# Optimization experiments

Measured on AMD Instinct MI355X. Metric: run time of the kernel, lower is better.

## Reference

```python
import jax, jax.numpy as jnp
import numpy as np

# 24 directional shifts (dy, dx): out[h,w] = in[h-dy, w-dx], zero elsewhere.
SHIFTS = [(0,1),(0,-1),(1,0),(-1,0),(1,1),(-1,-1),(1,-1),(-1,1),
          (0,2),(0,-2),(2,0),(-2,0),(2,2),(-2,-2),(2,-2),(-2,2),
          (2,1),(1,2),(2,-1),(1,-2),(-2,1),(-1,2),(-2,-1),(-1,-2)]

def shift2d(xg, dy, dx):
    B, G, H, W = xg.shape
    pt, pb = max(dy,0), max(-dy,0)
    pl, pr = max(dx,0), max(-dx,0)
    xp = jnp.pad(xg, ((0,0),(0,0),(pt,pb),(pl,pr)))
    return xp[:, :, pb:pb+H, pr:pr+W]

def mul_shift(x4, gamma=1.0/24.0):
    B, C, H, W = x4.shape
    g = int(C * gamma)
    parts = [shift2d(x4[:, i*g:(i+1)*g], dy, dx) for i, (dy, dx) in enumerate(SHIFTS)]
    parts.append(x4[:, 24*g:])
    return jnp.concatenate(parts, axis=1)

def zigzag_indices(h, w, start='top-left', direction='horizontal'):
    if start == 'top-left':   row_start, col_start, row_step, col_step = 0, 0, 1, 1
    elif start == 'top-right': row_start, col_start, row_step, col_step = 0, w-1, 1, -1
    elif start == 'bottom-left': row_start, col_start, row_step, col_step = h-1, 0, -1, 1
    else:                     row_start, col_start, row_step, col_step = h-1, w-1, -1, -1
    idx = []
    for i in range(h):
        r = row_start + row_step * i
        if direction == 'horizontal':
            cols = range(w) if r % 2 == 0 else range(w-1, -1, -1)
            idx += [r * w + c for c in cols]
        else:
            cc = col_start + col_step * i
            rows = range(h) if cc % 2 == 0 else range(h-1, -1, -1)
            idx += [rr * w + cc for rr in rows]
    return np.asarray(idx, dtype=np.int32)

def wkv(w, u, k, v):
    """Numerically stable RWKV WKV recurrence. w,u:(C,) k,v:(B,T,C) -> (B,T,C)."""
    B, T, C = k.shape
    def step(carry, kv):
        p, q, o = carry
        kt, vt = kv
        no = jnp.maximum(o, u + kt)
        A = jnp.exp(o - no); Bc = jnp.exp(u + kt - no)
        y = (A * p + Bc * vt) / (A * q + Bc)
        no2 = jnp.maximum(w + o, kt)
        A2 = jnp.exp(w + o - no2); B2 = jnp.exp(kt - no2)
        return (A2 * p + B2 * vt, A2 * q + B2, no2), y
    init = (jnp.zeros((B, C), k.dtype), jnp.zeros((B, C), k.dtype),
            jnp.full((B, C), -1e38, k.dtype))
    _, ys = jax.lax.scan(step, init, (jnp.swapaxes(k, 0, 1), jnp.swapaxes(v, 0, 1)))
    return jnp.swapaxes(ys, 0, 1)

def setup_inputs() -> dict:
    key = jax.random.key(0)
    ks = jax.random.split(key, 8)
    B, H, W, C = 8, 64, 64, 768
    scale = 0.02
    return {
        'x': jax.random.normal(ks[0], (B, H*W, C), jnp.float32),
        'key_w': jax.random.normal(ks[1], (C, C), jnp.float32) * scale,
        'value_w': jax.random.normal(ks[2], (C, C), jnp.float32) * scale,
        'receptance_w': jax.random.normal(ks[3], (C, C), jnp.float32) * scale,
        'output_w': jax.random.normal(ks[4], (C, C), jnp.float32) * scale,
        'spatial_decay': jax.random.normal(ks[5], (2, C), jnp.float32),
        'spatial_first': jax.random.normal(ks[6], (2, C), jnp.float32),
        'h': H, 'w': W,
    }

def reference(x, key_w, value_w, receptance_w, output_w, spatial_decay, spatial_first, h, w):
    B, T, C = x.shape
    # layer_id=0 -> scheme ('top-left','horizontal')
    order = jnp.asarray(zigzag_indices(h, w, 'top-left', 'horizontal'))
    inv = jnp.argsort(order)
    # jit_func: mul_shift in (B,C,H,W), zigzag reorder along T, projections
    x4 = jnp.transpose(x.reshape(B, h, w, C), (0, 3, 1, 2))
    x4 = mul_shift(x4)
    xs = jnp.transpose(x4.reshape(B, C, T)[:, :, order], (0, 2, 1))  # (B,T,C)
    k = xs @ key_w.T
    v = xs @ value_w.T
    sr = jax.nn.sigmoid(xs @ receptance_w.T)
    # recurrence j=0
    v = wkv(spatial_decay[0] / T, spatial_first[0] / T, k, v)
    # recurrence j=1: zigzag-permute, WKV, inverse-permute (horizontal -> same grid)
    k2 = k[:, order]
    v2 = v[:, order]
    v2 = wkv(spatial_decay[1] / T, spatial_first[1] / T, k2, v2)
    v = v2[:, inv]
    return (sr * v) @ output_w.T
```

## Files before the change

### kernel.cpp

```cpp
#include <hip/hip_runtime.h>
#include <hip/hip_bf16.h>
#include <hip/hip_fp16.h>

#define T_SEQ 4096
#define CDIM  768
#define BDIM  8
#define MROWS (BDIM * T_SEQ)
#define NKVR  (3 * CDIM)
#define CHL   32
#define NCH   (T_SEQ / CHL)
#define BC    (BDIM * CDIM)

typedef __attribute__((ext_vector_type(8))) short   short8;
typedef __attribute__((ext_vector_type(4))) float   floatx4;
typedef unsigned short ushort_t;
typedef unsigned int   uint_t;
struct ushort4_t { ushort_t x, y, z, w; };

__device__ __forceinline__ ushort_t f2b(float f) {
    __hip_bfloat16 h = __float2bfloat16(f);
    return *(ushort_t*)&h;
}
__device__ __forceinline__ float b2f(ushort_t s) {
    __hip_bfloat16 h;
    *(ushort_t*)&h = s;
    return __bfloat162float(h);
}
__device__ __forceinline__ ushort_t f2h(float f) {
    __half h = __float2half(f);
    return *(ushort_t*)&h;
}
__device__ __forceinline__ float h2f(ushort_t s) {
    __half h;
    *(ushort_t*)&h = s;
    return __half2float(h);
}

__device__ __forceinline__ void gload_lds16(const void* g, void* l) {
    __builtin_amdgcn_global_load_lds(
        (const __attribute__((address_space(1))) void*)g,
        (__attribute__((address_space(3))) void*)l, 16, 0, 0);
}

__constant__ int c_dy[24] = {0,0,1,-1,1,-1,1,-1,0,0,2,-2,2,-2,2,-2,2,1,2,1,-2,-1,-2,-1};
__constant__ int c_dx[24] = {1,-1,0,0,1,-1,-1,1,2,-2,0,0,2,-2,-2,2,1,2,-1,-2,1,2,-1,-2};

__global__ void cvt_weights(const float* __restrict__ kw, const float* __restrict__ vw,
                            const float* __restrict__ rw, const float* __restrict__ ow,
                            ushort_t* __restrict__ wkvr, ushort_t* __restrict__ wo) {
    int i = blockIdx.x * 256 + threadIdx.x;
    if (i < CDIM * CDIM) {
        wkvr[i]                   = f2b(kw[i]);
        wkvr[i + CDIM * CDIM]     = f2b(vw[i]);
        wkvr[i + 2 * CDIM * CDIM] = f2b(rw[i]);
        wo[i]                     = f2b(ow[i]);
    }
}

__global__ void shift_zigzag(const float* __restrict__ x, ushort_t* __restrict__ xs) {
    size_t i = (size_t)blockIdx.x * 256 + threadIdx.x;
    if (i >= (size_t)MROWS * (CDIM / 4)) return;
    int c4 = (int)(i % (CDIM / 4)) * 4;
    size_t bt = i / (CDIM / 4);
    int tz = (int)(bt % T_SEQ);
    int b  = (int)(bt / T_SEQ);
    int r = tz >> 6, pos = tz & 63;
    int xcol = (r & 1) ? (63 - pos) : pos;
    int g = c4 >> 5;
    int ys = r - c_dy[g];
    int xsrc = xcol - c_dx[g];
    float4 val = {0.f, 0.f, 0.f, 0.f};
    if ((unsigned)ys < 64u && (unsigned)xsrc < 64u)
        val = *(const float4*)(x + ((size_t)b * T_SEQ + (size_t)(ys * 64 + xsrc)) * CDIM + c4);
    ushort4_t o;
    o.x = f2b(val.x); o.y = f2b(val.y); o.z = f2b(val.z); o.w = f2b(val.w);
    *(ushort4_t*)(xs + bt * CDIM + c4) = o;
}

template <int MODE, int NB>
__global__ __launch_bounds__(256, 3) void gemm_bt(
    const ushort_t* __restrict__ A, const ushort_t* __restrict__ Bw,
    ushort_t* __restrict__ kbuf, ushort_t* __restrict__ vbuf,
    ushort_t* __restrict__ out_sr, float* __restrict__ out_f) {
    __shared__ ushort_t As[128 * 64];
    __shared__ ushort_t Bs[128 * 64];
    const int p    = blockIdx.x;
    const int xcd  = p & 7;
    const int s    = p >> 3;
    const int mb   = xcd + 8 * (s / NB);
    const int nb   = s % NB;
    const int m0   = mb * 128;
    const int n0   = nb * 128;
    const int t    = threadIdx.x;
    const int lane = t & 63;
    const int wv   = t >> 6;
    const int wm   = (wv & 1) * 64;
    const int wn   = (wv >> 1) * 64;
    const int srow = t >> 3;
    const int sch  = t & 7;
    const int l15  = lane & 15;
    const int l4   = lane >> 4;

    floatx4 acc[4][4];
#pragma unroll
    for (int i = 0; i < 4; i++)
#pragma unroll
        for (int j = 0; j < 4; j++) acc[i][j] = (floatx4){0.f, 0.f, 0.f, 0.f};

    for (int kk = 0; kk < CDIM; kk += 64) {
        __syncthreads();
#pragma unroll
        for (int j = 0; j < 4; j++) {
            const int rowA = 32 * j + srow;
            const int gc   = sch ^ (rowA & 7);
            gload_lds16(A  + (size_t)(m0 + rowA) * CDIM + kk + gc * 8,
                        (void*)(As + j * 2048 + t * 8));
            gload_lds16(Bw + (size_t)(n0 + rowA) * CDIM + kk + gc * 8,
                        (void*)(Bs + j * 2048 + t * 8));
        }
        __syncthreads();
#pragma unroll
        for (int k2 = 0; k2 < 2; k2++) {
            short8 af[4], bfv[4];
#pragma unroll
            for (int mi = 0; mi < 4; mi++) {
                int ra = wm + mi * 16 + l15;
                int c  = k2 * 4 + l4;
                af[mi] = *(const short8*)(As + ra * 64 + ((c ^ (ra & 7)) << 3));
            }
#pragma unroll
            for (int ni = 0; ni < 4; ni++) {
                int rb = wn + ni * 16 + l15;
                int c  = k2 * 4 + l4;
                bfv[ni] = *(const short8*)(Bs + rb * 64 + ((c ^ (rb & 7)) << 3));
            }
#pragma unroll
            for (int mi = 0; mi < 4; mi++)
#pragma unroll
                for (int ni = 0; ni < 4; ni++)
                    acc[mi][ni] = __builtin_amdgcn_mfma_f32_16x16x32_bf16(
                        af[mi], bfv[ni], acc[mi][ni], 0, 0, 0);
        }
    }

    const int region = (MODE == 0) ? (nb / 6) : 0;
    const int ncb = n0 - region * CDIM;
#pragma unroll
    for (int mi = 0; mi < 4; mi++) {
#pragma unroll
        for (int ni = 0; ni < 4; ni++) {
            int nc = ncb + wn + ni * 16 + l15;
#pragma unroll
            for (int r = 0; r < 4; r++) {
                int mg = m0 + wm + mi * 16 + l4 * 4 + r;
                float val = acc[mi][ni][r];
                if (MODE == 0) {
                    if (region == 0)
                        kbuf[(size_t)mg * CDIM + nc] = f2h(val);
                    else if (region == 1)
                        vbuf[(size_t)mg * CDIM + nc] = f2h(val);
                    else
                        out_sr[(size_t)mg * CDIM + nc] =
                            f2b(1.0f / (1.0f + __expf(-val)));
                } else {
                    out_f[(size_t)mg * CDIM + (n0 + wn + ni * 16 + l15)] = val;
                }
            }
        }
    }
}


__global__ __launch_bounds__(256) void wkv_chunk_sum0(
    const ushort_t* __restrict__ kb, const ushort_t* __restrict__ vb,
    const float* __restrict__ sd,
    float* __restrict__ sumP, float* __restrict__ sumQ, float* __restrict__ sumO) {
    int gid = blockIdx.x * 256 + threadIdx.x;
    int bc = gid % BC;
    int ch = gid / BC;
    int b = bc / CDIM, c = bc % CDIM;
    const float w = sd[c] * (1.0f / (float)T_SEQ);
    const size_t base = ((size_t)b * T_SEQ + ch * CHL) * CDIM + c;
    const ushort_t* kp = kb + base;
    const ushort_t* vp = vb + base;
    float p = 0.f, q = 0.f, o = -1e38f;
#pragma unroll 8
    for (int i = 0; i < CHL; i++) {
        float kt = h2f(kp[(size_t)i * CDIM]), vt = h2f(vp[(size_t)i * CDIM]);
        float wo_ = w + o;
        float no2 = fmaxf(wo_, kt);
        float A2 = __expf(wo_ - no2), B2 = __expf(kt - no2);
        p = A2 * p + B2 * vt;
        q = A2 * q + B2;
        o = no2;
    }
    size_t idx = (size_t)ch * BC + bc;
    sumP[idx] = p; sumQ[idx] = q; sumO[idx] = o;
}

__global__ __launch_bounds__(256) void wkv_chunk_scan(
    const float* __restrict__ sumP, const float* __restrict__ sumQ,
    const float* __restrict__ sumO,
    float* __restrict__ inP, float* __restrict__ inQ, float* __restrict__ inO,
    const float* __restrict__ sd, int pass) {
    int bc = blockIdx.x * 256 + threadIdx.x;
    if (bc >= BC) return;
    int c = bc % CDIM;
    const float w = sd[pass * CDIM + c] * (1.0f / (float)T_SEQ);
    const float Lw = w * (float)CHL;
    float p = 0.f, q = 0.f, o = -1e38f;
    for (int ch = 0; ch < NCH; ch++) {
        size_t idx = (size_t)ch * BC + bc;
        inP[idx] = p; inQ[idx] = q; inO[idx] = o;
        float Pc = sumP[idx], Qc = sumQ[idx], Oc = sumO[idx];
        float ow_ = o + Lw;
        float no = fmaxf(ow_, Oc);
        float e1 = __expf(ow_ - no), e2 = __expf(Oc - no);
        p = e1 * p + e2 * Pc;
        q = e1 * q + e2 * Qc;
        o = no;
    }
}

__global__ __launch_bounds__(256) void wkv_replay0_sum1(
    const ushort_t* __restrict__ kb, ushort_t* __restrict__ vb,
    const float* __restrict__ sd, const float* __restrict__ sf,
    const float* __restrict__ inP, const float* __restrict__ inQ,
    const float* __restrict__ inO,
    float* __restrict__ sumP, float* __restrict__ sumQ, float* __restrict__ sumO) {
    int gid = blockIdx.x * 256 + threadIdx.x;
    int bc = gid % BC;
    int ch = gid / BC;
    int b = bc / CDIM, c = bc % CDIM;
    const float w1 = sd[c] * (1.0f / (float)T_SEQ);
    const float u1 = sf[c] * (1.0f / (float)T_SEQ);
    const size_t base = ((size_t)b * T_SEQ + ch * CHL) * CDIM + c;
    const ushort_t* kp = kb + base;
    ushort_t* vp = vb + base;
    size_t idx = (size_t)ch * BC + bc;
    float p = inP[idx], q = inQ[idx], o = inO[idx];
    float yv[CHL];
    float kvk[CHL];
#pragma unroll
    for (int i = 0; i < CHL; i++) {
        float kt = h2f(kp[(size_t)i * CDIM]), vt = h2f(vp[(size_t)i * CDIM]);
        kvk[i] = kt;
        float uk = u1 + kt;
        float no = fmaxf(o, uk);
        float Ae = __expf(o - no), Be = __expf(uk - no);
        float y = (Ae * p + Be * vt) / (Ae * q + Be);
        float wo_ = w1 + o;
        float no2 = fmaxf(wo_, kt);
        float A2 = __expf(wo_ - no2), B2 = __expf(kt - no2);
        p = A2 * p + B2 * vt;
        q = A2 * q + B2;
        o = no2;
        yv[i] = y;
        vp[(size_t)i * CDIM] = f2h(y);
    }
    const float w2 = sd[CDIM + c] * (1.0f / (float)T_SEQ);
    float p2 = 0.f, q2 = 0.f, o2 = -1e38f;
    const bool rev = (ch >> 1) & 1;
#pragma unroll
    for (int j = 0; j < CHL; j++) {
        int i = rev ? (CHL - 1 - j) : j;
        float kt = kvk[i], vt = yv[i];
        float wo_ = w2 + o2;
        float no2 = fmaxf(wo_, kt);
        float A2 = __expf(wo_ - no2), B2 = __expf(kt - no2);
        p2 = A2 * p2 + B2 * vt;
        q2 = A2 * q2 + B2;
        o2 = no2;
    }
    size_t idx2 = (size_t)((ch & 2) ? (ch ^ 1) : ch) * BC + bc;
    sumP[idx2] = p2; sumQ[idx2] = q2; sumO[idx2] = o2;
}

__global__ __launch_bounds__(256) void wkv_replay1(
    const ushort_t* __restrict__ kb, const ushort_t* __restrict__ vb,
    const ushort_t* __restrict__ srb, ushort_t* __restrict__ a2,
    const float* __restrict__ sd, const float* __restrict__ sf,
    const float* __restrict__ inP, const float* __restrict__ inQ,
    const float* __restrict__ inO) {
    int gid = blockIdx.x * 256 + threadIdx.x;
    int bc = gid % BC;
    int ch = gid / BC;
    int b = bc / CDIM, c = bc % CDIM;
    const float w = sd[CDIM + c] * (1.0f / (float)T_SEQ);
    const float u = sf[CDIM + c] * (1.0f / (float)T_SEQ);
    size_t base = (size_t)b * T_SEQ * CDIM + c;
    size_t idx = (size_t)ch * BC + bc;
    float p = inP[idx], q = inQ[idx], o = inO[idx];
    const int r = ch >> 1;
    const int pos0 = (ch & 1) * CHL;
#pragma unroll 8
    for (int i = 0; i < CHL; i++) {
        int pos = pos0 + i;
        int col = (r & 1) ? (63 - pos) : pos;
        size_t off = base + (size_t)(r * 64 + col) * CDIM;
        float kt = h2f(kb[off]), vt = h2f(vb[off]);
        float uk = u + kt;
        float no = fmaxf(o, uk);
        float Ae = __expf(o - no), Be = __expf(uk - no);
        float y = (Ae * p + Be * vt) / (Ae * q + Be);
        float wo_ = w + o;
        float no2 = fmaxf(wo_, kt);
        float A2 = __expf(wo_ - no2), B2 = __expf(kt - no2);
        p = A2 * p + B2 * vt;
        q = A2 * q + B2;
        o = no2;
        a2[off] = f2b(y * b2f(srb[off]));
    }
}

extern "C" void kernel_launch(void* const* d_in, const int* in_sizes, int n_in,
                              void* d_out, int out_size, void* d_ws, size_t ws_size,
                              hipStream_t stream) {
    (void)in_sizes; (void)n_in; (void)out_size; (void)ws_size;
    const float* x  = (const float*)d_in[0];
    const float* kw = (const float*)d_in[1];
    const float* vw = (const float*)d_in[2];
    const float* rw = (const float*)d_in[3];
    const float* ow = (const float*)d_in[4];
    const float* sd = (const float*)d_in[5];
    const float* sf = (const float*)d_in[6];
    float* out = (float*)d_out;

    char* ws = (char*)d_ws;
    size_t off = 0;
    auto alloc = [&](size_t bytes) -> void* {
        void* p = ws + off;
        off += (bytes + 255) & ~(size_t)255;
        return p;
    };
    ushort_t* xs   = (ushort_t*)alloc((size_t)MROWS * CDIM * 2);
    ushort_t* kb   = (ushort_t*)alloc((size_t)MROWS * CDIM * 2);
    ushort_t* vb   = (ushort_t*)alloc((size_t)MROWS * CDIM * 2);
    ushort_t* srb  = (ushort_t*)alloc((size_t)MROWS * CDIM * 2);
    ushort_t* wkvr = (ushort_t*)alloc((size_t)NKVR * CDIM * 2);
    ushort_t* wo   = (ushort_t*)alloc((size_t)CDIM * CDIM * 2);
    float*    sumP = (float*)   alloc((size_t)NCH * BC * 4);
    float*    sumQ = (float*)   alloc((size_t)NCH * BC * 4);
    float*    sumO = (float*)   alloc((size_t)NCH * BC * 4);
    float*    inP  = (float*)   alloc((size_t)NCH * BC * 4);
    float*    inQ  = (float*)   alloc((size_t)NCH * BC * 4);
    float*    inO  = (float*)   alloc((size_t)NCH * BC * 4);

    cvt_weights<<<(CDIM * CDIM + 255) / 256, 256, 0, stream>>>(kw, vw, rw, ow, wkvr, wo);
    shift_zigzag<<<(int)(((size_t)MROWS * (CDIM / 4) + 255) / 256), 256, 0, stream>>>(x, xs);
    gemm_bt<0, 18><<<(MROWS / 128) * (NKVR / 128), 256, 0, stream>>>(
        xs, wkvr, kb, vb, srb, nullptr);

    const int nwkv = NCH * BC;
    wkv_chunk_sum0<<<nwkv / 256, 256, 0, stream>>>(kb, vb, sd, sumP, sumQ, sumO);
    wkv_chunk_scan<<<(BC + 255) / 256, 256, 0, stream>>>(sumP, sumQ, sumO,
                                                         inP, inQ, inO, sd, 0);
    wkv_replay0_sum1<<<nwkv / 256, 256, 0, stream>>>(kb, vb, sd, sf,
                                                     inP, inQ, inO, sumP, sumQ, sumO);
    wkv_chunk_scan<<<(BC + 255) / 256, 256, 0, stream>>>(sumP, sumQ, sumO,
                                                         inP, inQ, inO, sd, 1);
    wkv_replay1<<<nwkv / 256, 256, 0, stream>>>(kb, vb, srb, xs,
                                                sd, sf, inP, inQ, inO);

    gemm_bt<1, 6><<<(MROWS / 128) * (CDIM / 128), 256, 0, stream>>>(
        xs, wo, nullptr, nullptr, nullptr, out);
}
```

Baseline: 566.6 us.

## Store k/v/sr in channel-major layout for vectorized contiguous WKV chunk access

The first GEMM now writes the k, v and sigmoid(r) planes transposed as (B, C, T), packing four consecutive time steps per store. This lets every WKV chunk kernel load its 32-step chunk with wide short8 loads instead of strided per-element reads. The chunk-summary buffers become channel-major too, and the shift kernel now handles 8 channels per thread. The cost is strided transposed stores in the GEMM epilogue and more registers in the fully unrolled WKV kernels.

```diff
diff --git a/kernel.cpp b/kernel.cpp
--- a/kernel.cpp
+++ b/kernel.cpp
@@ -15,7 +15,6 @@
 typedef __attribute__((ext_vector_type(4))) float   floatx4;
 typedef unsigned short ushort_t;
 typedef unsigned int   uint_t;
-struct ushort4_t { ushort_t x, y, z, w; };
 
 __device__ __forceinline__ ushort_t f2b(float f) {
     __hip_bfloat16 h = __float2bfloat16(f);
@@ -59,29 +58,34 @@
 
 __global__ void shift_zigzag(const float* __restrict__ x, ushort_t* __restrict__ xs) {
     size_t i = (size_t)blockIdx.x * 256 + threadIdx.x;
-    if (i >= (size_t)MROWS * (CDIM / 4)) return;
-    int c4 = (int)(i % (CDIM / 4)) * 4;
-    size_t bt = i / (CDIM / 4);
+    int c8 = (int)(i % (CDIM / 8)) * 8;
+    size_t bt = i / (CDIM / 8);
     int tz = (int)(bt % T_SEQ);
     int b  = (int)(bt / T_SEQ);
     int r = tz >> 6, pos = tz & 63;
     int xcol = (r & 1) ? (63 - pos) : pos;
-    int g = c4 >> 5;
+    int g = c8 >> 5;
     int ys = r - c_dy[g];
     int xsrc = xcol - c_dx[g];
-    float4 val = {0.f, 0.f, 0.f, 0.f};
-    if ((unsigned)ys < 64u && (unsigned)xsrc < 64u)
-        val = *(const float4*)(x + ((size_t)b * T_SEQ + (size_t)(ys * 64 + xsrc)) * CDIM + c4);
-    ushort4_t o;
-    o.x = f2b(val.x); o.y = f2b(val.y); o.z = f2b(val.z); o.w = f2b(val.w);
-    *(ushort4_t*)(xs + bt * CDIM + c4) = o;
+    float4 v0 = {0.f, 0.f, 0.f, 0.f}, v1 = {0.f, 0.f, 0.f, 0.f};
+    if ((unsigned)ys < 64u && (unsigned)xsrc < 64u) {
+        const float* src = x + ((size_t)b * T_SEQ + (size_t)(ys * 64 + xsrc)) * CDIM + c8;
+        v0 = *(const float4*)(src);
+        v1 = *(const float4*)(src + 4);
+    }
+    short8 o;
+    o[0] = (short)f2b(v0.x); o[1] = (short)f2b(v0.y);
+    o[2] = (short)f2b(v0.z); o[3] = (short)f2b(v0.w);
+    o[4] = (short)f2b(v1.x); o[5] = (short)f2b(v1.y);
+    o[6] = (short)f2b(v1.z); o[7] = (short)f2b(v1.w);
+    *(short8*)(xs + bt * CDIM + c8) = o;
 }
 
 template <int MODE, int NB>
-__global__ __launch_bounds__(256, 3) void gemm_bt(
+__device__ __forceinline__ void gemm_body(
     const ushort_t* __restrict__ A, const ushort_t* __restrict__ Bw,
     ushort_t* __restrict__ kbuf, ushort_t* __restrict__ vbuf,
-    ushort_t* __restrict__ out_sr, float* __restrict__ out_f) {
+    ushort_t* __restrict__ srbuf, float* __restrict__ out_f) {
     __shared__ ushort_t As[128 * 64];
     __shared__ ushort_t Bs[128 * 64];
     const int p    = blockIdx.x;
@@ -143,31 +147,59 @@
         }
     }
 
-    const int region = (MODE == 0) ? (nb / 6) : 0;
-    const int ncb = n0 - region * CDIM;
-#pragma unroll
-    for (int mi = 0; mi < 4; mi++) {
-#pragma unroll
-        for (int ni = 0; ni < 4; ni++) {
-            int nc = ncb + wn + ni * 16 + l15;
-#pragma unroll
-            for (int r = 0; r < 4; r++) {
-                int mg = m0 + wm + mi * 16 + l4 * 4 + r;
-                float val = acc[mi][ni][r];
-                if (MODE == 0) {
-                    if (region == 0)
-                        kbuf[(size_t)mg * CDIM + nc] = f2h(val);
-                    else if (region == 1)
-                        vbuf[(size_t)mg * CDIM + nc] = f2h(val);
-                    else
-                        out_sr[(size_t)mg * CDIM + nc] =
-                            f2b(1.0f / (1.0f + __expf(-val)));
+    if (MODE == 0) {
+        const int region = nb / 6;
+        const int ncb = n0 - region * CDIM;
+        const int bidx = mb >> 5;
+        const int tt   = (mb & 31) * 128;
+        ushort_t* plane = (region == 0) ? kbuf : (region == 1) ? vbuf : srbuf;
+#pragma unroll
+        for (int mi = 0; mi < 4; mi++) {
+#pragma unroll
+            for (int ni = 0; ni < 4; ni++) {
+                const int nc = ncb + wn + ni * 16 + l15;
+                const int t0 = tt + wm + mi * 16 + l4 * 4;
+                uint_t lo, hi;
+                if (region == 2) {
+                    lo = (uint_t)f2b(1.0f / (1.0f + __expf(-acc[mi][ni][0]))) |
+                         ((uint_t)f2b(1.0f / (1.0f + __expf(-acc[mi][ni][1]))) << 16);
+                    hi = (uint_t)f2b(1.0f / (1.0f + __expf(-acc[mi][ni][2]))) |
+                         ((uint_t)f2b(1.0f / (1.0f + __expf(-acc[mi][ni][3]))) << 16);
                 } else {
-                    out_f[(size_t)mg * CDIM + (n0 + wn + ni * 16 + l15)] = val;
+                    lo = (uint_t)f2h(acc[mi][ni][0]) | ((uint_t)f2h(acc[mi][ni][1]) << 16);
+                    hi = (uint_t)f2h(acc[mi][ni][2]) | ((uint_t)f2h(acc[mi][ni][3]) << 16);
+                }
+                uint2 pk = make_uint2(lo, hi);
+                *(uint2*)(plane + ((size_t)bidx * CDIM + nc) * T_SEQ + t0) = pk;
+            }
+        }
+    } else {
+#pragma unroll
+        for (int mi = 0; mi < 4; mi++) {
+#pragma unroll
+            for (int ni = 0; ni < 4; ni++) {
+                const int nc = n0 + wn + ni * 16 + l15;
+#pragma unroll
+                for (int r = 0; r < 4; r++) {
+                    const int mg = m0 + wm + mi * 16 + l4 * 4 + r;
+                    out_f[(size_t)mg * CDIM + nc] = acc[mi][ni][r];
                 }
             }
         }
     }
+}
+
+__global__ __launch_bounds__(256, 3) void gemm_kvr(
+    const ushort_t* __restrict__ A, const ushort_t* __restrict__ Bw,
+    ushort_t* __restrict__ kbuf, ushort_t* __restrict__ vbuf,
+    ushort_t* __restrict__ srbuf) {
+    gemm_body<0, 18>(A, Bw, kbuf, vbuf, srbuf, nullptr);
+}
+
+__global__ __launch_bounds__(256, 3) void gemm_out(
+    const ushort_t* __restrict__ A, const ushort_t* __restrict__ Bw,
+    float* __restrict__ out_f) {
+    gemm_body<1, 6>(A, Bw, nullptr, nullptr, nullptr, out_f);
 }
 
 
@@ -176,17 +208,20 @@
     const float* __restrict__ sd,
     float* __restrict__ sumP, float* __restrict__ sumQ, float* __restrict__ sumO) {
     int gid = blockIdx.x * 256 + threadIdx.x;
-    int bc = gid % BC;
-    int ch = gid / BC;
-    int b = bc / CDIM, c = bc % CDIM;
+    int ch = gid & (NCH - 1);
+    int bc = gid >> 7;
+    int c = bc % CDIM;
     const float w = sd[c] * (1.0f / (float)T_SEQ);
-    const size_t base = ((size_t)b * T_SEQ + ch * CHL) * CDIM + c;
-    const ushort_t* kp = kb + base;
-    const ushort_t* vp = vb + base;
+    const short8* kp = (const short8*)(kb + (size_t)bc * T_SEQ + ch * CHL);
+    const short8* vp = (const short8*)(vb + (size_t)bc * T_SEQ + ch * CHL);
+    short8 ks[4], vs[4];
+#pragma unroll
+    for (int r = 0; r < 4; r++) { ks[r] = kp[r]; vs[r] = vp[r]; }
     float p = 0.f, q = 0.f, o = -1e38f;
-#pragma unroll 8
+#pragma unroll
     for (int i = 0; i < CHL; i++) {
-        float kt = h2f(kp[(size_t)i * CDIM]), vt = h2f(vp[(size_t)i * CDIM]);
+        float kt = h2f((ushort_t)ks[i >> 3][i & 7]);
+        float vt = h2f((ushort_t)vs[i >> 3][i & 7]);
         float wo_ = w + o;
         float no2 = fmaxf(wo_, kt);
         float A2 = __expf(wo_ - no2), B2 = __expf(kt - no2);
@@ -194,7 +229,7 @@
         q = A2 * q + B2;
         o = no2;
     }
-    size_t idx = (size_t)ch * BC + bc;
+    size_t idx = (size_t)bc * NCH + ch;
     sumP[idx] = p; sumQ[idx] = q; sumO[idx] = o;
 }
 
@@ -208,11 +243,17 @@
     int c = bc % CDIM;
     const float w = sd[pass * CDIM + c] * (1.0f / (float)T_SEQ);
     const float Lw = w * (float)CHL;
+    const float* sp = sumP + (size_t)bc * NCH;
+    const float* sq = sumQ + (size_t)bc * NCH;
+    const float* so = sumO + (size_t)bc * NCH;
+    float* ip = inP + (size_t)bc * NCH;
+    float* iq = inQ + (size_t)bc * NCH;
+    float* io = inO + (size_t)bc * NCH;
     float p = 0.f, q = 0.f, o = -1e38f;
+#pragma unroll 4
     for (int ch = 0; ch < NCH; ch++) {
-        size_t idx = (size_t)ch * BC + bc;
-        inP[idx] = p; inQ[idx] = q; inO[idx] = o;
-        float Pc = sumP[idx], Qc = sumQ[idx], Oc = sumO[idx];
+        ip[ch] = p; iq[ch] = q; io[ch] = o;
+        float Pc = sp[ch], Qc = sq[ch], Oc = so[ch];
         float ow_ = o + Lw;
         float no = fmaxf(ow_, Oc);
         float e1 = __expf(ow_ - no), e2 = __expf(Oc - no);
@@ -231,20 +272,21 @@
     int gid = blockIdx.x * 256 + threadIdx.x;
     int bc = gid % BC;
     int ch = gid / BC;
-    int b = bc / CDIM, c = bc % CDIM;
+    int c = bc % CDIM;
     const float w1 = sd[c] * (1.0f / (float)T_SEQ);
     const float u1 = sf[c] * (1.0f / (float)T_SEQ);
-    const size_t base = ((size_t)b * T_SEQ + ch * CHL) * CDIM + c;
-    const ushort_t* kp = kb + base;
-    ushort_t* vp = vb + base;
-    size_t idx = (size_t)ch * BC + bc;
-    float p = inP[idx], q = inQ[idx], o = inO[idx];
-    float yv[CHL];
-    float kvk[CHL];
+    const size_t base = (size_t)bc * T_SEQ + ch * CHL;
+    const short8* kp = (const short8*)(kb + base);
+    short8* vp = (short8*)(vb + base);
+    short8 ks[4], vs[4], ys[4];
+#pragma unroll
+    for (int r = 0; r < 4; r++) { ks[r] = kp[r]; vs[r] = vp[r]; }
+    size_t sidx = (size_t)bc * NCH + ch;
+    float p = inP[sidx], q = inQ[sidx], o = inO[sidx];
 #pragma unroll
     for (int i = 0; i < CHL; i++) {
-        float kt = h2f(kp[(size_t)i * CDIM]), vt = h2f(vp[(size_t)i * CDIM]);
-        kvk[i] = kt;
+        float kt = h2f((ushort_t)ks[i >> 3][i & 7]);
+        float vt = h2f((ushort_t)vs[i >> 3][i & 7]);
         float uk = u1 + kt;
         float no = fmaxf(o, uk);
         float Ae = __expf(o - no), Be = __expf(uk - no);
@@ -255,25 +297,34 @@
         p = A2 * p + B2 * vt;
         q = A2 * q + B2;
         o = no2;
-        yv[i] = y;
-        vp[(size_t)i * CDIM] = f2h(y);
-    }
+        ys[i >> 3][i & 7] = (short)f2h(y);
+    }
+#pragma unroll
+    for (int r = 0; r < 4; r++) vp[r] = ys[r];
     const float w2 = sd[CDIM + c] * (1.0f / (float)T_SEQ);
     float p2 = 0.f, q2 = 0.f, o2 = -1e38f;
-    const bool rev = (ch >> 1) & 1;
-#pragma unroll
-    for (int j = 0; j < CHL; j++) {
-        int i = rev ? (CHL - 1 - j) : j;
-        float kt = kvk[i], vt = yv[i];
-        float wo_ = w2 + o2;
-        float no2 = fmaxf(wo_, kt);
-        float A2 = __expf(wo_ - no2), B2 = __expf(kt - no2);
-        p2 = A2 * p2 + B2 * vt;
-        q2 = A2 * q2 + B2;
-        o2 = no2;
-    }
-    size_t idx2 = (size_t)((ch & 2) ? (ch ^ 1) : ch) * BC + bc;
-    sumP[idx2] = p2; sumQ[idx2] = q2; sumO[idx2] = o2;
+#define P2STEP(IDX)                                                         \
+    {                                                                       \
+        float kt = h2f((ushort_t)ks[(IDX) >> 3][(IDX) & 7]);                \
+        float yt = h2f((ushort_t)ys[(IDX) >> 3][(IDX) & 7]);                \
+        float wo_ = w2 + o2;                                                \
+        float nn = fmaxf(wo_, kt);                                          \
+        float A2 = __expf(wo_ - nn), B2 = __expf(kt - nn);                  \
+        p2 = A2 * p2 + B2 * yt;                                             \
+        q2 = A2 * q2 + B2;                                                  \
+        o2 = nn;                                                            \
+    }
+    if (((ch >> 1) & 1) == 0) {
+#pragma unroll
+        for (int j = 0; j < CHL; j++) P2STEP(j)
+    } else {
+#pragma unroll
+        for (int j = 0; j < CHL; j++) P2STEP(CHL - 1 - j)
+    }
+#undef P2STEP
+    int idx2 = (ch & 2) ? (ch ^ 1) : ch;
+    size_t oidx = (size_t)bc * NCH + idx2;
+    sumP[oidx] = p2; sumQ[oidx] = q2; sumO[oidx] = o2;
 }
 
 __global__ __launch_bounds__(256) void wkv_replay1(
@@ -288,29 +339,44 @@
     int b = bc / CDIM, c = bc % CDIM;
     const float w = sd[CDIM + c] * (1.0f / (float)T_SEQ);
     const float u = sf[CDIM + c] * (1.0f / (float)T_SEQ);
-    size_t base = (size_t)b * T_SEQ * CDIM + c;
-    size_t idx = (size_t)ch * BC + bc;
-    float p = inP[idx], q = inQ[idx], o = inO[idx];
     const int r = ch >> 1;
     const int pos0 = (ch & 1) * CHL;
-#pragma unroll 8
-    for (int i = 0; i < CHL; i++) {
-        int pos = pos0 + i;
-        int col = (r & 1) ? (63 - pos) : pos;
-        size_t off = base + (size_t)(r * 64 + col) * CDIM;
-        float kt = h2f(kb[off]), vt = h2f(vb[off]);
-        float uk = u + kt;
-        float no = fmaxf(o, uk);
-        float Ae = __expf(o - no), Be = __expf(uk - no);
-        float y = (Ae * p + Be * vt) / (Ae * q + Be);
-        float wo_ = w + o;
-        float no2 = fmaxf(wo_, kt);
-        float A2 = __expf(wo_ - no2), B2 = __expf(kt - no2);
-        p = A2 * p + B2 * vt;
-        q = A2 * q + B2;
-        o = no2;
-        a2[off] = f2b(y * b2f(srb[off]));
-    }
+    const int t_lo = r * 64 + ((r & 1) ? (CHL - pos0) : pos0);
+    const size_t base = (size_t)bc * T_SEQ + t_lo;
+    const short8* kp = (const short8*)(kb + base);
+    const short8* vp = (const short8*)(vb + base);
+    const short8* sp = (const short8*)(srb + base);
+    short8 ks[4], vs[4], ss[4];
+#pragma unroll
+    for (int rr = 0; rr < 4; rr++) { ks[rr] = kp[rr]; vs[rr] = vp[rr]; ss[rr] = sp[rr]; }
+    size_t sidx = (size_t)bc * NCH + ch;
+    float p = inP[sidx], q = inQ[sidx], o = inO[sidx];
+    ushort_t* aout = a2 + ((size_t)b * T_SEQ + t_lo) * CDIM + c;
+#define R1STEP(E)                                                           \
+    {                                                                       \
+        float kt = h2f((ushort_t)ks[(E) >> 3][(E) & 7]);                    \
+        float vt = h2f((ushort_t)vs[(E) >> 3][(E) & 7]);                    \
+        float uk = u + kt;                                                  \
+        float no = fmaxf(o, uk);                                            \
+        float Ae = __expf(o - no), Be = __expf(uk - no);                    \
+        float y = (Ae * p + Be * vt) / (Ae * q + Be);                       \
+        float wo_ = w + o;                                                  \
+        float nn = fmaxf(wo_, kt);                                          \
+        float A2 = __expf(wo_ - nn), B2 = __expf(kt - nn);                  \
+        p = A2 * p + B2 * vt;                                               \
+        q = A2 * q + B2;                                                    \
+        o = nn;                                                             \
+        aout[(size_t)(E) * CDIM] =                                          \
+            f2b(y * b2f((ushort_t)ss[(E) >> 3][(E) & 7]));                  \
+    }
+    if ((r & 1) == 0) {
+#pragma unroll
+        for (int j = 0; j < CHL; j++) R1STEP(j)
+    } else {
+#pragma unroll
+        for (int j = 0; j < CHL; j++) R1STEP(CHL - 1 - j)
+    }
+#undef R1STEP
 }
 
 extern "C" void kernel_launch(void* const* d_in, const int* in_sizes, int n_in,
@@ -347,9 +413,9 @@
     float*    inO  = (float*)   alloc((size_t)NCH * BC * 4);
 
     cvt_weights<<<(CDIM * CDIM + 255) / 256, 256, 0, stream>>>(kw, vw, rw, ow, wkvr, wo);
-    shift_zigzag<<<(int)(((size_t)MROWS * (CDIM / 4) + 255) / 256), 256, 0, stream>>>(x, xs);
-    gemm_bt<0, 18><<<(MROWS / 128) * (NKVR / 128), 256, 0, stream>>>(
-        xs, wkvr, kb, vb, srb, nullptr);
+    shift_zigzag<<<(int)((size_t)MROWS * (CDIM / 8) / 256), 256, 0, stream>>>(x, xs);
+    gemm_kvr<<<(MROWS / 128) * (NKVR / 128), 256, 0, stream>>>(
+        xs, wkvr, kb, vb, srb);
 
     const int nwkv = NCH * BC;
     wkv_chunk_sum0<<<nwkv / 256, 256, 0, stream>>>(kb, vb, sd, sumP, sumQ, sumO);
@@ -362,6 +428,5 @@
     wkv_replay1<<<nwkv / 256, 256, 0, stream>>>(kb, vb, srb, xs,
                                                 sd, sf, inP, inQ, inO);
 
-    gemm_bt<1, 6><<<(MROWS / 128) * (CDIM / 128), 256, 0, stream>>>(
-        xs, wo, nullptr, nullptr, nullptr, out);
-}
+    gemm_out<<<(MROWS / 128) * (CDIM / 128), 256, 0, stream>>>(xs, wo, out);
+}
```

Result: slower. 582.0 us (+2.7%).
